# Kernel optimization log

Hardware: AMD Instinct MI355X
Metric: run time of the kernel (lower is better)

The kernel has to match this reference:

```python
import jax, jax.numpy as jnp
import numpy as np

HEADS = 8
EPS = 1e-5


def _layernorm(x, g, b):
    mu = jnp.mean(x, axis=-1, keepdims=True)
    var = jnp.mean(jnp.square(x - mu), axis=-1, keepdims=True)
    return (x - mu) * jax.lax.rsqrt(var + EPS) * g + b


def setup_inputs() -> dict:
    key = jax.random.key(0)
    ks = jax.random.split(key, 10)
    B, S, D = 4, 2048, 256
    d_ff = 2 * D
    s = 0.02
    return {
        "x": jax.random.normal(ks[0], (B, S, D), dtype=jnp.float32),
        "ln1_g": jnp.ones((D,), jnp.float32),
        "ln1_b": jnp.zeros((D,), jnp.float32),
        "w_qkv": jax.random.normal(ks[1], (3 * D, D), jnp.float32) * s,
        "b_qkv": jnp.zeros((3 * D,), jnp.float32),
        "w_proj": jax.random.normal(ks[2], (D, D), jnp.float32) * s,
        "b_proj": jnp.zeros((D,), jnp.float32),
        "ln2_g": jnp.ones((D,), jnp.float32),
        "ln2_b": jnp.zeros((D,), jnp.float32),
        "w1": jax.random.normal(ks[3], (d_ff, D), jnp.float32) * s,
        "b1": jnp.zeros((d_ff,), jnp.float32),
        "w2": jax.random.normal(ks[4], (D, d_ff), jnp.float32) * s,
        "b2": jnp.zeros((D,), jnp.float32),
    }


def reference(x, ln1_g, ln1_b, w_qkv, b_qkv, w_proj, b_proj,
              ln2_g, ln2_b, w1, b1, w2, b2):
    B, S, D = x.shape
    H = HEADS
    dh = D // H
    scale = dh ** -0.5

    # --- attention sublayer (pre-LN) ---
    y = _layernorm(x, ln1_g, ln1_b)
    qkv = y @ w_qkv.T + b_qkv                       # [B,S,3D]
    qkv = qkv.reshape(B, S, 3, H, dh)
    q = jnp.transpose(qkv[:, :, 0], (0, 2, 1, 3))   # [B,H,S,dh]
    k = jnp.transpose(qkv[:, :, 1], (0, 2, 1, 3))
    v = jnp.transpose(qkv[:, :, 2], (0, 2, 1, 3))
    attn = jax.nn.softmax(jnp.einsum('bhsd,bhtd->bhst', q, k) * scale, axis=-1)
    ctx = jnp.einsum('bhst,bhtd->bhsd', attn, v)    # [B,H,S,dh]
    ctx = jnp.transpose(ctx, (0, 2, 1, 3)).reshape(B, S, D)
    x = x + ctx @ w_proj.T + b_proj

    # --- FFN sublayer (pre-LN) ---
    y = _layernorm(x, ln2_g, ln2_b)
    h = jax.nn.silu(y @ w1.T + b1)                  # [B,S,2D]
    x = x + h @ w2.T + b2
    return x
```

## Files before the change

kernel.cpp:

```cpp
#include <hip/hip_runtime.h>
#include <cstddef>

constexpr int kB   = 4;
constexpr int kS   = 2048;
constexpr int kD   = 256;
constexpr int kH   = 8;
constexpr int kDH  = 32;
constexpr int kDFF = 512;
constexpr int kM   = kB * kS;
constexpr float kEps = 1e-5f;
constexpr float kScaleL2E = 0.17677669529663687f * 1.4426950408889634f;

typedef float f32x4  __attribute__((ext_vector_type(4)));
typedef short bf16x8 __attribute__((ext_vector_type(8)));
typedef unsigned short u16;
typedef unsigned int   u32;

__device__ inline u16 f2bf(float x) {
    union { float f; unsigned u; } c; c.f = x;
    const unsigned r = c.u + 0x7fffu + ((c.u >> 16) & 1u);
    return (u16)(r >> 16);
}

__device__ inline u32 pk_trunc(float lo, float hi) {
    union { float f; u32 u; } a, b; a.f = lo; b.f = hi;
    return __builtin_amdgcn_perm(b.u, a.u, 0x07060302u);
}

__global__ __launch_bounds__(256)
void ln_kernel(const float* __restrict__ x, const float* __restrict__ g,
               const float* __restrict__ b, u16* __restrict__ y)
{
    const int wave = threadIdx.x >> 6;
    const int lane = threadIdx.x & 63;
    const int row  = blockIdx.x * 4 + wave;
    const float4 v = *(const float4*)&x[(size_t)row * kD + lane * 4];
    float s1 = (v.x + v.y) + (v.z + v.w);
    float s2 = (v.x * v.x + v.y * v.y) + (v.z * v.z + v.w * v.w);
    #pragma unroll
    for (int off = 1; off < 64; off <<= 1) {
        s1 += __shfl_xor(s1, off);
        s2 += __shfl_xor(s2, off);
    }
    const float mu  = s1 * (1.0f / kD);
    const float var = s2 * (1.0f / kD) - mu * mu;
    const float inv = rsqrtf(var + kEps);
    const float4 g4 = *(const float4*)&g[lane * 4];
    const float4 b4 = *(const float4*)&b[lane * 4];
    *(ushort4*)&y[(size_t)row * kD + lane * 4] = make_ushort4(
        f2bf((v.x - mu) * inv * g4.x + b4.x),
        f2bf((v.y - mu) * inv * g4.y + b4.y),
        f2bf((v.z - mu) * inv * g4.z + b4.z),
        f2bf((v.w - mu) * inv * g4.w + b4.w));
}

template<int NT, int OUTMODE, bool RES, int KTOT>
__global__ __launch_bounds__(256, 3)
void gemm_bf16(const u16* __restrict__ A, const float* __restrict__ Wf,
               const float* __restrict__ bias, const float* __restrict__ res,
               float* __restrict__ Cf, u16* __restrict__ Cb,
               u16* __restrict__ KbP, u16* __restrict__ VtP, int N)
{
    constexpr int BSTR = KTOT + 4;
    constexpr int NI   = NT / 16;
    constexpr int NK   = KTOT / 32;
    __shared__ u16 Bs[NT * BSTR];
    const int tid  = threadIdx.x;
    const int wave = tid >> 6;
    const int lane = tid & 63;
    const int quad = lane >> 4;
    const int l16  = lane & 15;
    const int m0 = blockIdx.x * 128;
    const int n0 = blockIdx.y * NT;

    {
        constexpr int ITS = (NT * KTOT) / 1024;
        #pragma unroll
        for (int it = 0; it < ITS; ++it) {
            const int e   = it * 1024 + tid * 4;
            const int row = e / KTOT;
            const int col = e & (KTOT - 1);
            const float4 wv = *(const float4*)&Wf[(size_t)(n0 + row) * KTOT + col];
            *(ushort4*)&Bs[row * BSTR + col] = make_ushort4(
                f2bf(wv.x), f2bf(wv.y), f2bf(wv.z), f2bf(wv.w));
        }
    }
    __syncthreads();

    bf16x8 wfr[NI][NK];
    #pragma unroll
    for (int ni = 0; ni < NI; ++ni)
        #pragma unroll
        for (int k = 0; k < NK; ++k)
            wfr[ni][k] = *(const bf16x8*)
                &Bs[(ni * 16 + l16) * BSTR + k * 32 + quad * 8];

    f32x4 acc[2][NI];
    #pragma unroll
    for (int mt = 0; mt < 2; ++mt)
        #pragma unroll
        for (int ni = 0; ni < NI; ++ni) acc[mt][ni] = {0.f, 0.f, 0.f, 0.f};

    const u16* arow0 = &A[(size_t)(m0 + wave * 16 + l16) * KTOT];
    const u16* arow1 = &A[(size_t)(m0 + 64 + wave * 16 + l16) * KTOT];

    #pragma unroll
    for (int k = 0; k < NK; ++k) {
        const bf16x8 a0 = *(const bf16x8*)&arow0[k * 32 + quad * 8];
        const bf16x8 a1 = *(const bf16x8*)&arow1[k * 32 + quad * 8];
        #pragma unroll
        for (int ni = 0; ni < NI; ++ni) {
            acc[0][ni] = __builtin_amdgcn_mfma_f32_16x16x32_bf16(a0, wfr[ni][k], acc[0][ni], 0, 0, 0);
            acc[1][ni] = __builtin_amdgcn_mfma_f32_16x16x32_bf16(a1, wfr[ni][k], acc[1][ni], 0, 0, 0);
        }
    }

    #pragma unroll
    for (int mt = 0; mt < 2; ++mt) {
        #pragma unroll
        for (int ni = 0; ni < NI; ++ni) {
            const float bias_v = bias[n0 + ni * 16 + l16];
            #pragma unroll
            for (int r = 0; r < 4; ++r) {
                const int m = m0 + mt * 64 + wave * 16 + quad * 4 + r;
                float v = acc[mt][ni][r] + bias_v;
                if (OUTMODE == 0) {
                    const int n = n0 + ni * 16 + l16;
                    if (RES) v += res[(size_t)m * N + n];
                    Cf[(size_t)m * N + n] = v;
                } else if (OUTMODE == 1) {
                    const int n = n0 + ni * 16 + l16;
                    v = v / (1.0f + __expf(-v));
                    Cb[(size_t)m * N + n] = f2bf(v);
                } else {
                    const int rgn = n0 >> 8;
                    const int nl  = (n0 & 255) + ni * 16 + l16;
                    const int hh  = nl >> 5, dh = nl & 31;
                    const int bb  = m >> 11, s = m & (kS - 1);
                    const int bh  = bb * kH + hh;
                    if (rgn == 0)
                        Cb[((size_t)bh * kS + s) * kDH + dh] = f2bf(v * kScaleL2E);
                    else if (rgn == 1)
                        KbP[((size_t)bh * kS + s) * kDH + dh] = f2bf(v);
                    else {
                        const int so = s & 31;
                        const int vq = (so >> 2) & 3;
                        const int vj = (so & 3) | (((so >> 4) & 1) << 2);
                        VtP[(((size_t)bh * (kS / 32) + (s >> 5)) * 4 + vq) * 256
                            + dh * 8 + vj] = f2bf(v);
                    }
                }
            }
        }
    }
}

__global__ __launch_bounds__(256)
void attn_kernel(const u16* __restrict__ Qb, const u16* __restrict__ Kb,
                 const u16* __restrict__ Vp, u16* __restrict__ ctx)
{
    __shared__ float cbuf[2][64 * 33];
    const int tid  = threadIdx.x;
    const int wave = tid >> 6;
    const int lane = tid & 63;
    const int quad = lane >> 4;
    const int l16  = lane & 15;
    const int h = blockIdx.y;
    const int b = blockIdx.z;
    const int bh = b * kH + h;
    const int qsub = wave >> 1;
    const int half = wave & 1;
    const int q0 = blockIdx.x * 128 + qsub * 64;

    bf16x8 aq[4];
    #pragma unroll
    for (int qb = 0; qb < 4; ++qb)
        aq[qb] = *(const bf16x8*)
            &Qb[((size_t)bh * kS + q0 + qb * 16 + l16) * kDH + quad * 8];

    const u16* Kbase = Kb + (size_t)bh * kS * kDH;
    const u16* Vbase = Vp + (size_t)bh * (kS * 32);

    f32x4 O[4][2] = {};
    f32x4 lsum[4] = {};
    const f32x4 zz = {0.f, 0.f, 0.f, 0.f};
    union { u32 u[4]; bf16x8 v; } ones;
    ones.u[0] = ones.u[1] = ones.u[2] = ones.u[3] = 0x3F803F80u;

    auto load_tile = [&](int kt, bf16x8 (&kf)[4], bf16x8 (&vf)[2][2]) {
        #pragma unroll
        for (int kg = 0; kg < 4; ++kg)
            kf[kg] = *(const bf16x8*)
                &Kbase[(size_t)(kt + kg * 16 + l16) * kDH + quad * 8];
        #pragma unroll
        for (int ks = 0; ks < 2; ++ks)
            #pragma unroll
            for (int nf = 0; nf < 2; ++nf)
                vf[ks][nf] = *(const bf16x8*)
                    &Vbase[(size_t)(((kt >> 5) + ks) * 4 + quad) * 1024
                           + (nf * 16 + l16) * 8];
    };

    auto comp_tile = [&](bf16x8 (&kf)[4], bf16x8 (&vf)[2][2]) {
        #pragma unroll
        for (int qb = 0; qb < 4; ++qb) {
            f32x4 S0 = __builtin_amdgcn_mfma_f32_16x16x32_bf16(kf[0], aq[qb], zz, 0, 0, 0);
            f32x4 S1 = __builtin_amdgcn_mfma_f32_16x16x32_bf16(kf[1], aq[qb], zz, 0, 0, 0);
            f32x4 S2 = __builtin_amdgcn_mfma_f32_16x16x32_bf16(kf[2], aq[qb], zz, 0, 0, 0);
            f32x4 S3 = __builtin_amdgcn_mfma_f32_16x16x32_bf16(kf[3], aq[qb], zz, 0, 0, 0);

            union { u32 u[4]; bf16x8 v; } pA0, pA1;
            pA0.u[0] = pk_trunc(__builtin_amdgcn_exp2f(S0[0]), __builtin_amdgcn_exp2f(S0[1]));
            pA0.u[1] = pk_trunc(__builtin_amdgcn_exp2f(S0[2]), __builtin_amdgcn_exp2f(S0[3]));
            pA0.u[2] = pk_trunc(__builtin_amdgcn_exp2f(S1[0]), __builtin_amdgcn_exp2f(S1[1]));
            pA0.u[3] = pk_trunc(__builtin_amdgcn_exp2f(S1[2]), __builtin_amdgcn_exp2f(S1[3]));
            pA1.u[0] = pk_trunc(__builtin_amdgcn_exp2f(S2[0]), __builtin_amdgcn_exp2f(S2[1]));
            pA1.u[1] = pk_trunc(__builtin_amdgcn_exp2f(S2[2]), __builtin_amdgcn_exp2f(S2[3]));
            pA1.u[2] = pk_trunc(__builtin_amdgcn_exp2f(S3[0]), __builtin_amdgcn_exp2f(S3[1]));
            pA1.u[3] = pk_trunc(__builtin_amdgcn_exp2f(S3[2]), __builtin_amdgcn_exp2f(S3[3]));

            lsum[qb] = __builtin_amdgcn_mfma_f32_16x16x32_bf16(pA0.v, ones.v, lsum[qb], 0, 0, 0);
            lsum[qb] = __builtin_amdgcn_mfma_f32_16x16x32_bf16(pA1.v, ones.v, lsum[qb], 0, 0, 0);

            O[qb][0] = __builtin_amdgcn_mfma_f32_16x16x32_bf16(pA0.v, vf[0][0], O[qb][0], 0, 0, 0);
            O[qb][1] = __builtin_amdgcn_mfma_f32_16x16x32_bf16(pA0.v, vf[0][1], O[qb][1], 0, 0, 0);
            O[qb][0] = __builtin_amdgcn_mfma_f32_16x16x32_bf16(pA1.v, vf[1][0], O[qb][0], 0, 0, 0);
            O[qb][1] = __builtin_amdgcn_mfma_f32_16x16x32_bf16(pA1.v, vf[1][1], O[qb][1], 0, 0, 0);
        }
    };

    const int kbeg = half * (kS / 2);
    #pragma unroll 1
    for (int t2 = 0; t2 < 8; ++t2) {
        const int ktA = kbeg + t2 * 128;
        bf16x8 kfA[4], vfA[2][2], kfB[4], vfB[2][2];
        load_tile(ktA,      kfA, vfA);
        load_tile(ktA + 64, kfB, vfB);
        comp_tile(kfA, vfA);
        comp_tile(kfB, vfB);
    }

    float* cb = cbuf[qsub];
    if (half == 1) {
        #pragma unroll
        for (int qb = 0; qb < 4; ++qb)
            #pragma unroll
            for (int r = 0; r < 4; ++r) {
                const int row = qb * 16 + quad * 4 + r;
                cb[row * 33 + l16]      = O[qb][0][r];
                cb[row * 33 + 16 + l16] = O[qb][1][r];
                if (l16 == 0)
                    cb[row * 33 + 32] = lsum[qb][r];
            }
    }
    __syncthreads();
    if (half == 0) {
        #pragma unroll
        for (int qb = 0; qb < 4; ++qb)
            #pragma unroll
            for (int r = 0; r < 4; ++r) {
                const int row = qb * 16 + quad * 4 + r;
                const float lq  = lsum[qb][r] + cb[row * 33 + 32];
                const float inv = 1.0f / lq;
                const float o0 = O[qb][0][r] + cb[row * 33 + l16];
                const float o1 = O[qb][1][r] + cb[row * 33 + 16 + l16];
                const int q = q0 + row;
                u16* crow = ctx + ((size_t)(b * kS + q)) * kD + h * kDH;
                crow[l16]      = f2bf(o0 * inv);
                crow[16 + l16] = f2bf(o1 * inv);
            }
    }
}

extern "C" void kernel_launch(void* const* d_in, const int* in_sizes, int n_in,
                              void* d_out, int out_size, void* d_ws, size_t ws_size,
                              hipStream_t stream)
{
    const float* x      = (const float*)d_in[0];
    const float* ln1_g  = (const float*)d_in[1];
    const float* ln1_b  = (const float*)d_in[2];
    const float* w_qkv  = (const float*)d_in[3];
    const float* b_qkv  = (const float*)d_in[4];
    const float* w_proj = (const float*)d_in[5];
    const float* b_proj = (const float*)d_in[6];
    const float* ln2_g  = (const float*)d_in[7];
    const float* ln2_b  = (const float*)d_in[8];
    const float* w1     = (const float*)d_in[9];
    const float* b1     = (const float*)d_in[10];
    const float* w2     = (const float*)d_in[11];
    const float* b2     = (const float*)d_in[12];
    float* out = (float*)d_out;

    char* ws = (char*)d_ws;
    u16* Qb  = (u16*)ws;
    u16* Kb  = (u16*)(ws + ((size_t)4  << 20));
    u16* Vp  = (u16*)(ws + ((size_t)8  << 20));
    u16* ctx = (u16*)(ws + ((size_t)12 << 20));
    u16* y   = (u16*)(ws + ((size_t)16 << 20));
    u16* h   = (u16*)ws;

    const dim3 blk(256);

    ln_kernel<<<dim3(kM / 4), blk, 0, stream>>>(x, ln1_g, ln1_b, y);
    gemm_bf16<32, 2, false, 256><<<dim3(kM / 128, 24), blk, 0, stream>>>(
        y, w_qkv, b_qkv, nullptr, nullptr, Qb, Kb, Vp, 0);
    attn_kernel<<<dim3(kS / 128, kH, kB), blk, 0, stream>>>(Qb, Kb, Vp, ctx);
    gemm_bf16<32, 0, true, 256><<<dim3(kM / 128, kD / 32), blk, 0, stream>>>(
        ctx, w_proj, b_proj, x, out, nullptr, nullptr, nullptr, kD);
    ln_kernel<<<dim3(kM / 4), blk, 0, stream>>>(out, ln2_g, ln2_b, y);
    gemm_bf16<32, 1, false, 256><<<dim3(kM / 128, kDFF / 32), blk, 0, stream>>>(
        y, w1, b1, nullptr, nullptr, h, nullptr, nullptr, kDFF);
    gemm_bf16<16, 0, true, 512><<<dim3(kM / 128, kD / 16), blk, 0, stream>>>(
        h, w2, b2, out, out, nullptr, nullptr, nullptr, kD);
}
```

Baseline: 172.9 us.

## Pre-convert weights to bf16 once and stream weight fragments directly from global

Adds a single kernel that converts all four weight matrices to bf16 into workspace, replacing the per-block fp32 load, convert and LDS staging in every GEMM block. The GEMM now reads bf16 weight fragments straight from global memory inside the k-loop, with no shared memory and no barrier. N-tiles grow (64 for QKV and W1, 32 for W2), which halves the grid in those launches. This adds one extra launch and relies on L2 caching for weight reuse across blocks, in exchange for removing redundant conversion and LDS traffic.

```diff
diff --git a/kernel.cpp b/kernel.cpp
--- a/kernel.cpp
+++ b/kernel.cpp
@@ -25,6 +25,22 @@
 __device__ inline u32 pk_trunc(float lo, float hi) {
     union { float f; u32 u; } a, b; a.f = lo; b.f = hi;
     return __builtin_amdgcn_perm(b.u, a.u, 0x07060302u);
+}
+
+__global__ __launch_bounds__(256)
+void conv_w_kernel(const float* __restrict__ wq, const float* __restrict__ wp,
+                   const float* __restrict__ w1, const float* __restrict__ w2,
+                   u16* __restrict__ dst)
+{
+    const int e0 = (blockIdx.x * 256 + threadIdx.x) * 4;
+    const float* src;
+    int off;
+    if (e0 < 196608)      { src = wq; off = e0; }
+    else if (e0 < 262144) { src = wp; off = e0 - 196608; }
+    else if (e0 < 393216) { src = w1; off = e0 - 262144; }
+    else                  { src = w2; off = e0 - 393216; }
+    const float4 v = *(const float4*)&src[off];
+    *(ushort4*)&dst[e0] = make_ushort4(f2bf(v.x), f2bf(v.y), f2bf(v.z), f2bf(v.w));
 }
 
 __global__ __launch_bounds__(256)
@@ -55,16 +71,14 @@
 }
 
 template<int NT, int OUTMODE, bool RES, int KTOT>
-__global__ __launch_bounds__(256, 3)
-void gemm_bf16(const u16* __restrict__ A, const float* __restrict__ Wf,
-               const float* __restrict__ bias, const float* __restrict__ res,
-               float* __restrict__ Cf, u16* __restrict__ Cb,
-               u16* __restrict__ KbP, u16* __restrict__ VtP, int N)
-{
-    constexpr int BSTR = KTOT + 4;
-    constexpr int NI   = NT / 16;
-    constexpr int NK   = KTOT / 32;
-    __shared__ u16 Bs[NT * BSTR];
+__global__ __launch_bounds__(256)
+void gemm_direct(const u16* __restrict__ A, const u16* __restrict__ Wb,
+                 const float* __restrict__ bias, const float* __restrict__ res,
+                 float* __restrict__ Cf, u16* __restrict__ Cb,
+                 u16* __restrict__ KbP, u16* __restrict__ VtP, int N)
+{
+    constexpr int NI = NT / 16;
+    constexpr int NK = KTOT / 32;
     const int tid  = threadIdx.x;
     const int wave = tid >> 6;
     const int lane = tid & 63;
@@ -73,45 +87,25 @@
     const int m0 = blockIdx.x * 128;
     const int n0 = blockIdx.y * NT;
 
-    {
-        constexpr int ITS = (NT * KTOT) / 1024;
-        #pragma unroll
-        for (int it = 0; it < ITS; ++it) {
-            const int e   = it * 1024 + tid * 4;
-            const int row = e / KTOT;
-            const int col = e & (KTOT - 1);
-            const float4 wv = *(const float4*)&Wf[(size_t)(n0 + row) * KTOT + col];
-            *(ushort4*)&Bs[row * BSTR + col] = make_ushort4(
-                f2bf(wv.x), f2bf(wv.y), f2bf(wv.z), f2bf(wv.w));
-        }
-    }
-    __syncthreads();
-
-    bf16x8 wfr[NI][NK];
-    #pragma unroll
-    for (int ni = 0; ni < NI; ++ni)
-        #pragma unroll
-        for (int k = 0; k < NK; ++k)
-            wfr[ni][k] = *(const bf16x8*)
-                &Bs[(ni * 16 + l16) * BSTR + k * 32 + quad * 8];
-
     f32x4 acc[2][NI];
     #pragma unroll
     for (int mt = 0; mt < 2; ++mt)
         #pragma unroll
         for (int ni = 0; ni < NI; ++ni) acc[mt][ni] = {0.f, 0.f, 0.f, 0.f};
 
-    const u16* arow0 = &A[(size_t)(m0 + wave * 16 + l16) * KTOT];
-    const u16* arow1 = &A[(size_t)(m0 + 64 + wave * 16 + l16) * KTOT];
-
-    #pragma unroll
+    const u16* arow0 = &A[(size_t)(m0 + wave * 16 + l16) * KTOT + quad * 8];
+    const u16* arow1 = &A[(size_t)(m0 + 64 + wave * 16 + l16) * KTOT + quad * 8];
+    const u16* wrow  = &Wb[(size_t)(n0 + l16) * KTOT + quad * 8];
+
+    #pragma unroll 2
     for (int k = 0; k < NK; ++k) {
-        const bf16x8 a0 = *(const bf16x8*)&arow0[k * 32 + quad * 8];
-        const bf16x8 a1 = *(const bf16x8*)&arow1[k * 32 + quad * 8];
+        const bf16x8 a0 = *(const bf16x8*)&arow0[k * 32];
+        const bf16x8 a1 = *(const bf16x8*)&arow1[k * 32];
         #pragma unroll
         for (int ni = 0; ni < NI; ++ni) {
-            acc[0][ni] = __builtin_amdgcn_mfma_f32_16x16x32_bf16(a0, wfr[ni][k], acc[0][ni], 0, 0, 0);
-            acc[1][ni] = __builtin_amdgcn_mfma_f32_16x16x32_bf16(a1, wfr[ni][k], acc[1][ni], 0, 0, 0);
+            const bf16x8 wf = *(const bf16x8*)&wrow[(size_t)ni * 16 * KTOT + k * 32];
+            acc[0][ni] = __builtin_amdgcn_mfma_f32_16x16x32_bf16(a0, wf, acc[0][ni], 0, 0, 0);
+            acc[1][ni] = __builtin_amdgcn_mfma_f32_16x16x32_bf16(a1, wf, acc[1][ni], 0, 0, 0);
         }
     }
 
@@ -298,18 +292,24 @@
     u16* ctx = (u16*)(ws + ((size_t)12 << 20));
     u16* y   = (u16*)(ws + ((size_t)16 << 20));
     u16* h   = (u16*)ws;
+    u16* Wb  = (u16*)(ws + ((size_t)20 << 20));
+    u16* wqb = Wb;
+    u16* wpb = Wb + 196608;
+    u16* w1b = Wb + 262144;
+    u16* w2b = Wb + 393216;
 
     const dim3 blk(256);
 
+    conv_w_kernel<<<dim3(512), blk, 0, stream>>>(w_qkv, w_proj, w1, w2, Wb);
     ln_kernel<<<dim3(kM / 4), blk, 0, stream>>>(x, ln1_g, ln1_b, y);
-    gemm_bf16<32, 2, false, 256><<<dim3(kM / 128, 24), blk, 0, stream>>>(
-        y, w_qkv, b_qkv, nullptr, nullptr, Qb, Kb, Vp, 0);
+    gemm_direct<64, 2, false, 256><<<dim3(kM / 128, 12), blk, 0, stream>>>(
+        y, wqb, b_qkv, nullptr, nullptr, Qb, Kb, Vp, 0);
     attn_kernel<<<dim3(kS / 128, kH, kB), blk, 0, stream>>>(Qb, Kb, Vp, ctx);
-    gemm_bf16<32, 0, true, 256><<<dim3(kM / 128, kD / 32), blk, 0, stream>>>(
-        ctx, w_proj, b_proj, x, out, nullptr, nullptr, nullptr, kD);
+    gemm_direct<32, 0, true, 256><<<dim3(kM / 128, kD / 32), blk, 0, stream>>>(
+        ctx, wpb, b_proj, x, out, nullptr, nullptr, nullptr, kD);
     ln_kernel<<<dim3(kM / 4), blk, 0, stream>>>(out, ln2_g, ln2_b, y);
-    gemm_bf16<32, 1, false, 256><<<dim3(kM / 128, kDFF / 32), blk, 0, stream>>>(
-        y, w1, b1, nullptr, nullptr, h, nullptr, nullptr, kDFF);
-    gemm_bf16<16, 0, true, 512><<<dim3(kM / 128, kD / 16), blk, 0, stream>>>(
-        h, w2, b2, out, out, nullptr, nullptr, nullptr, kD);
-}
+    gemm_direct<64, 1, false, 256><<<dim3(kM / 128, kDFF / 64), blk, 0, stream>>>(
+        y, w1b, b1, nullptr, nullptr, h, nullptr, nullptr, kDFF);
+    gemm_direct<32, 0, true, 512><<<dim3(kM / 128, kD / 32), blk, 0, stream>>>(
+        h, w2b, b2, out, out, nullptr, nullptr, nullptr, kD);
+}
```

After: 183.5 us. 6.1% more time.
